# Kernel optimization log

Hardware: AMD Instinct MI355X
Metric: run time of the kernel (lower is better)

Reference implementation:

```python
import jax, jax.numpy as jnp
import numpy as np


def setup_inputs() -> dict:
    key = jax.random.key(0)
    ks = iter(jax.random.split(key, 100))
    V3, Vm, K, E3, Em = 100000, 25000, 128, 800000, 200000
    c_in, c3, cm, c_out = 16, 128, 256, 21
    rn = lambda *s: jax.random.normal(next(ks), s, dtype=jnp.float32)
    ru = lambda *s: jax.random.uniform(next(ks), s, dtype=jnp.float32)
    ri = lambda hi, *s: jax.random.randint(next(ks), s, 0, hi)
    d = {}
    d['x_in'] = rn(1, V3, c_in)
    d['mass_3'] = ru(1, V3)
    d['evals_3'] = ru(1, K)
    d['evecs_3'] = rn(1, V3, K) * 0.01
    d['gX3_idx'] = ri(V3, E3, 2)
    d['gX3_val'] = rn(E3) * 0.05
    d['gY3_idx'] = ri(V3, E3, 2)
    d['gY3_val'] = rn(E3) * 0.05
    d['mass_m'] = ru(1, Vm)
    d['evals_m'] = ru(1, K)
    d['evecs_m'] = rn(1, Vm, K) * 0.01
    d['gXm_idx'] = ri(Vm, Em, 2)
    d['gXm_val'] = rn(Em) * 0.05
    d['gYm_idx'] = ri(Vm, Em, 2)
    d['gYm_val'] = rn(Em) * 0.05
    d['traces34'] = ri(Vm, V3)
    d['in_w'] = rn(c_in, c3) * 0.05
    d['in_b'] = rn(c3) * 0.05
    d['widen_w'] = rn(c3, cm) * 0.05
    d['widen_b'] = rn(cm) * 0.05
    d['narrow_w'] = rn(cm, c3) * 0.05
    d['narrow_b'] = rn(c3) * 0.05
    d['halve_w'] = rn(2 * c3, c3) * 0.05
    d['halve_b'] = rn(c3) * 0.05
    d['out_w'] = rn(c3, c_out) * 0.05
    d['out_b'] = rn(c_out) * 0.05
    for pre, C in (('enc', c3), ('mid', cm), ('dec', c3)):
        d[pre + '_dt'] = ru(2, C)
        d[pre + '_Are'] = rn(2, C, C) * 0.05
        d[pre + '_Aim'] = rn(2, C, C) * 0.05
        d[pre + '_w0'] = rn(2, 3 * C, C) * 0.05
        d[pre + '_b0'] = rn(2, C) * 0.05
        d[pre + '_w1'] = rn(2, C, C) * 0.05
        d[pre + '_b1'] = rn(2, C) * 0.05
        d[pre + '_w2'] = rn(2, C, C) * 0.05
        d[pre + '_b2'] = rn(2, C) * 0.05
    return d


def _spmm(idx, val, x, n):
    # sparse COO (n x n) @ x ; rows = idx[:,0], cols = idx[:,1]
    return jax.ops.segment_sum(val[:, None] * x[idx[:, 1]], idx[:, 0], num_segments=n)


def _block(x, mass, evals, evecs, gxi, gxv, gyi, gyv, dt, Are, Aim, w0, b0, w1, b1, w2, b2):
    # DiffusionNetBlock: spectral diffusion + rotated gradient features + MiniMLP + residual
    V = x.shape[1]
    x_spec = jnp.einsum('bvk,bvc->bkc', evecs, x * mass[..., None])          # to_basis
    coef = jnp.exp(-evals[..., None] * jnp.maximum(dt, 1e-8)[None, None, :])  # (B,K,C)
    xd = jnp.einsum('bvk,bkc->bvc', evecs, coef * x_spec)                     # from_basis
    gX = _spmm(gxi, gxv, xd[0], V)[None]                                      # (B,V,C)
    gY = _spmm(gyi, gyv, xd[0], V)[None]
    Br = gX @ Are - gY @ Aim                                                  # complex linear, with rotations
    Bi = gY @ Are + gX @ Aim
    gf = jnp.tanh(gX * Br + gY * Bi)                                          # inner product -> tanh
    h = jnp.concatenate([x, xd, gf], axis=-1)                                 # (B,V,3C)
    h = jax.nn.relu(h @ w0 + b0)
    h = jax.nn.relu(h @ w1 + b1)
    return (h @ w2 + b2) + x


def reference(x_in, mass_3, evals_3, evecs_3, gX3_idx, gX3_val, gY3_idx, gY3_val,
              mass_m, evals_m, evecs_m, gXm_idx, gXm_val, gYm_idx, gYm_val, traces34,
              in_w, in_b, enc_dt, enc_Are, enc_Aim, enc_w0, enc_b0, enc_w1, enc_b1, enc_w2, enc_b2,
              widen_w, widen_b, mid_dt, mid_Are, mid_Aim, mid_w0, mid_b0, mid_w1, mid_b1, mid_w2, mid_b2,
              narrow_w, narrow_b, halve_w, halve_b,
              dec_dt, dec_Are, dec_Aim, dec_w0, dec_b0, dec_w1, dec_b1, dec_w2, dec_b2,
              out_w, out_b):
    Vm = mass_m.shape[1]
    sl = lambda arrs, i: tuple(a[i] for a in arrs)
    enc_p = (enc_dt, enc_Are, enc_Aim, enc_w0, enc_b0, enc_w1, enc_b1, enc_w2, enc_b2)
    mid_p = (mid_dt, mid_Are, mid_Aim, mid_w0, mid_b0, mid_w1, mid_b1, mid_w2, mid_b2)
    dec_p = (dec_dt, dec_Are, dec_Aim, dec_w0, dec_b0, dec_w1, dec_b1, dec_w2, dec_b2)

    x3 = jax.nn.relu(x_in @ in_w + in_b)
    for i in range(enc_dt.shape[0]):
        x3 = _block(x3, mass_3, evals_3, evecs_3, gX3_idx, gX3_val, gY3_idx, gY3_val, *sl(enc_p, i))
    # scatter-max pooling fine -> coarse
    xm = jax.ops.segment_max(x3[0], traces34, num_segments=Vm)
    xm = jnp.where(jnp.isneginf(xm), 0.0, xm)[None]
    xm = jax.nn.relu(xm @ widen_w + widen_b)
    for i in range(mid_dt.shape[0]):
        xm = _block(xm, mass_m, evals_m, evecs_m, gXm_idx, gXm_val, gYm_idx, gYm_val, *sl(mid_p, i))
    # gather unpooling coarse -> fine
    y3 = xm[:, traces34, :]
    y3 = jax.nn.relu(y3 @ narrow_w + narrow_b)
    y3 = jnp.concatenate([y3, x3], axis=-1)
    y3 = jax.nn.relu(y3 @ halve_w + halve_b)
    for i in range(dec_dt.shape[0]):
        y3 = _block(y3, mass_3, evals_3, evecs_3, gX3_idx, gX3_val, gY3_idx, gY3_val, *sl(dec_p, i))
    return y3 @ out_w + out_b
```

## Files before the change

kernel.cpp:

```cpp
#include <hip/hip_runtime.h>
#include <cstdint>
#include <cstddef>

static constexpr int V3   = 100000;
static constexpr int VM   = 25000;
static constexpr int KE   = 128;
static constexpr int E3   = 800000;
static constexpr int EM   = 200000;
static constexpr int C3   = 128;
static constexpr int CMID = 256;

typedef unsigned short u16;
typedef unsigned int   u32;
using short8v = __attribute__((ext_vector_type(8))) short;
using f32x4   = __attribute__((ext_vector_type(4))) float;
using f32x16  = __attribute__((ext_vector_type(16))) float;

#define DEVI __device__ __forceinline__
DEVI float4 ld4(const float* p){ return *(const float4*)p; }
DEVI void   st4(float* p, float4 v){ *(float4*)p = v; }
DEVI float  bf2f(u16 u){ return __uint_as_float(((u32)u) << 16); }
DEVI u16    f2bf(float f){
  u32 u = __float_as_uint(f);
  u += 0x7FFFu + ((u >> 16) & 1u);
  return (u16)(u >> 16);
}
DEVI u32 pk2(float a, float b){ return (u32)f2bf(a) | ((u32)f2bf(b) << 16); }
DEVI short8v as8(uint4 v){ union { uint4 u; short8v s; } c; c.u = v; return c.s; }
DEVI int lofs(int row, int oct){ return row * 40 + ((oct ^ ((row >> 3) & 3)) << 3); }

static inline int cdiv(int a, int b){ return (a + b - 1) / b; }

template<bool RELU, bool RES, bool GATHER, bool OBF16>
__global__ __launch_bounds__(256)
void k_mgemm(const void* __restrict__ A0, int aty0, int K0,
             const u16* __restrict__ wt0, int wl0, int wo0,
             const void* __restrict__ A1, int aty1, int K1,
             const u16* __restrict__ wt1, int wl1, int wo1,
             const void* __restrict__ A2, int aty2, int K2,
             const u16* __restrict__ wt2, int wl2, int wo2,
             const int* __restrict__ gidx,
             const float* __restrict__ bias, const float* __restrict__ res,
             void* __restrict__ OUT, u16* __restrict__ OUTB, int CO, int V)
{
  __shared__ __align__(16) u16 As[64 * 40];
  __shared__ __align__(16) u16 Ws[128 * 40];

  const int tid  = threadIdx.x;
  const int wave = tid >> 6, lane = tid & 63;
  const int vbase = blockIdx.x * 64;
  const int ncol0 = blockIdx.y * 128;
  const int KT = K0 + K1 + K2;

  f32x4 acc[8];
  #pragma unroll
  for (int n = 0; n < 8; n++) { acc[n][0]=0.f; acc[n][1]=0.f; acc[n][2]=0.f; acc[n][3]=0.f; }

  const int ar = tid >> 2, ac = tid & 3;
  const int arow = vbase + ar;
  int grow0 = arow;
  if (GATHER && arow < V) grow0 = gidx[arow];

  for (int kt = 0; kt < KT; kt += 32) {
    {
      int kg = kt + ac * 8;
      uint4 aw = make_uint4(0,0,0,0);
      if (arow < V && kg < KT) {
        const void* src; int aty, koff, sK; bool s0;
        if (kg < K0)            { src=A0; aty=aty0; koff=0;     sK=K0; s0=true;  }
        else if (kg < K0 + K1)  { src=A1; aty=aty1; koff=K0;    sK=K1; s0=false; }
        else                    { src=A2; aty=aty2; koff=K0+K1; sK=K2; s0=false; }
        int row = (GATHER && s0) ? grow0 : arow;
        int kl = kg - koff;
        if (aty) {
          aw = *(const uint4*)((const u16*)src + (size_t)row * sK + kl);
        } else {
          const float* fp = (const float*)src + (size_t)row * sK + kl;
          float4 x = ld4(fp), y = ld4(fp + 4);
          aw = make_uint4(pk2(x.x,x.y), pk2(x.z,x.w), pk2(y.x,y.y), pk2(y.z,y.w));
        }
      }
      *(uint4*)&As[ar * 40 + ac * 8] = aw;
    }
    #pragma unroll
    for (int i = 0; i < 2; i++) {
      int col = tid & 127;
      int c = (tid >> 7) + 2 * i;
      int kg = kt + c * 8;
      uint4 ww = make_uint4(0,0,0,0);
      if (kg < KT) {
        const u16* wt; int koff, wl, wo;
        if (kg < K0)           { wt=wt0; koff=0;     wl=wl0; wo=wo0; }
        else if (kg < K0+K1)   { wt=wt1; koff=K0;    wl=wl1; wo=wo1; }
        else                   { wt=wt2; koff=K0+K1; wl=wl2; wo=wo2; }
        ww = *(const uint4*)(wt + (size_t)(ncol0 + col) * wl + wo + (kg - koff));
      }
      *(uint4*)&Ws[col * 40 + c * 8] = ww;
    }
    __syncthreads();
    {
      const int mrow = (wave << 4) + (lane & 15);
      const int kc = lane >> 4;
      short8v a = *(const short8v*)(const void*)&As[mrow * 40 + kc * 8];
      #pragma unroll
      for (int n = 0; n < 8; n++) {
        short8v b = *(const short8v*)(const void*)&Ws[(n * 16 + (lane & 15)) * 40 + kc * 8];
        acc[n] = __builtin_amdgcn_mfma_f32_16x16x32_bf16(a, b, acc[n], 0, 0, 0);
      }
    }
    __syncthreads();
  }

  const int q4 = (lane >> 4) * 4, colb = lane & 15;
  #pragma unroll
  for (int n = 0; n < 8; n++) {
    int gcol = ncol0 + n * 16 + colb;
    float bv = bias ? bias[gcol] : 0.f;
    #pragma unroll
    for (int q = 0; q < 4; q++) {
      int grow = vbase + (wave << 4) + q4 + q;
      if (grow >= V) continue;
      float o = acc[n][q] + bv;
      size_t idx = (size_t)grow * CO + gcol;
      if (RES) o += res[idx];
      if (RELU) o = fmaxf(o, 0.f);
      if (OBF16) ((u16*)OUT)[idx] = f2bf(o);
      else {
        ((float*)OUT)[idx] = o;
        if (OUTB) OUTB[idx] = f2bf(o);
      }
    }
  }
}

__global__ __launch_bounds__(256)
void k_mlp3(const u16* __restrict__ A0, const u16* __restrict__ A1,
            const u16* __restrict__ A2,
            const u16* __restrict__ w0t,
            const u16* __restrict__ w1t, const u16* __restrict__ w2t,
            const float* __restrict__ b0, const float* __restrict__ b1,
            const float* __restrict__ b2,
            float* __restrict__ XM, u16* __restrict__ SHB, int V)
{
  __shared__ __align__(16) u16 As[64 * 40];
  __shared__ __align__(16) u16 Ws[128 * 40];
  __shared__ __align__(16) u16 Hs[4][64 * 40];

  const int tid  = threadIdx.x;
  const int wave = tid >> 6, lane = tid & 63;
  const int vbase = blockIdx.x * 64;
  const int ar = tid >> 2, ac = tid & 3;
  const int arow = vbase + ar;
  const bool rok = arow < V;
  const int mrow = (wave << 4) + (lane & 15);
  const int kc = lane >> 4;
  const int q4 = (lane >> 4) * 4, colb = lane & 15;
  const int wcol = tid & 127, wc = tid >> 7;

  float xres[8][4];
  #pragma unroll
  for (int n = 0; n < 8; n++)
    #pragma unroll
    for (int q = 0; q < 4; q++) {
      int grow = vbase + (wave << 4) + q4 + q;
      xres[n][q] = (grow < V) ? XM[(size_t)grow * C3 + n * 16 + colb] : 0.f;
    }

  f32x4 acc[8];
  auto zacc = [&]{
    #pragma unroll
    for (int n = 0; n < 8; n++) { acc[n][0]=0.f; acc[n][1]=0.f; acc[n][2]=0.f; acc[n][3]=0.f; }
  };
  auto hwrite = [&](const float* b){
    #pragma unroll
    for (int n = 0; n < 8; n++) {
      int c = n * 16 + colb;
      float bv = b[c];
      #pragma unroll
      for (int q = 0; q < 4; q++) {
        int row = (wave << 4) + q4 + q;
        Hs[c >> 5][lofs(row, (c >> 3) & 3) + (c & 7)] = f2bf(fmaxf(acc[n][q] + bv, 0.f));
      }
    }
  };
  auto mfma_tile = [&](const u16* a8){
    short8v a = *(const short8v*)(const void*)a8;
    #pragma unroll
    for (int n = 0; n < 8; n++) {
      short8v b = *(const short8v*)(const void*)&Ws[(n * 16 + (lane & 15)) * 40 + kc * 8];
      acc[n] = __builtin_amdgcn_mfma_f32_16x16x32_bf16(a, b, acc[n], 0, 0, 0);
    }
  };
  auto fA = [&](int kg) -> uint4 {
    const u16* src = (kg < 128) ? A0 : (kg < 256) ? A1 : A2;
    uint4 r = make_uint4(0,0,0,0);
    if (rok) r = *(const uint4*)(src + (size_t)arow * 128 + (kg & 127));
    return r;
  };
  auto fW = [&](const u16* wt, int ld, int kg) -> uint4 {
    return *(const uint4*)(wt + (size_t)wcol * ld + kg);
  };

  zacc();
  uint4 pa  = fA(ac * 8);
  uint4 pw0 = fW(w0t, 384, wc * 8);
  uint4 pw1 = fW(w0t, 384, (wc + 2) * 8);
  for (int kt = 0; kt < 384; kt += 32) {
    __syncthreads();
    *(uint4*)&As[ar * 40 + ac * 8] = pa;
    *(uint4*)&Ws[wcol * 40 + wc * 8] = pw0;
    *(uint4*)&Ws[wcol * 40 + (wc + 2) * 8] = pw1;
    __syncthreads();
    int kn = kt + 32;
    if (kn < 384) {
      pa  = fA(kn + ac * 8);
      pw0 = fW(w0t, 384, kn + wc * 8);
      pw1 = fW(w0t, 384, kn + (wc + 2) * 8);
    } else {
      pw0 = fW(w1t, 128, wc * 8);
      pw1 = fW(w1t, 128, (wc + 2) * 8);
    }
    mfma_tile(&As[mrow * 40 + kc * 8]);
  }
  hwrite(b0);
  zacc();
  for (int kt = 0; kt < 128; kt += 32) {
    __syncthreads();
    *(uint4*)&Ws[wcol * 40 + wc * 8] = pw0;
    *(uint4*)&Ws[wcol * 40 + (wc + 2) * 8] = pw1;
    __syncthreads();
    int kn = kt + 32;
    if (kn < 128) {
      pw0 = fW(w1t, 128, kn + wc * 8);
      pw1 = fW(w1t, 128, kn + (wc + 2) * 8);
    } else {
      pw0 = fW(w2t, 128, wc * 8);
      pw1 = fW(w2t, 128, (wc + 2) * 8);
    }
    mfma_tile(&Hs[kt >> 5][lofs(mrow, kc)]);
  }
  hwrite(b1);
  zacc();
  for (int kt = 0; kt < 128; kt += 32) {
    __syncthreads();
    *(uint4*)&Ws[wcol * 40 + wc * 8] = pw0;
    *(uint4*)&Ws[wcol * 40 + (wc + 2) * 8] = pw1;
    __syncthreads();
    int kn = kt + 32;
    if (kn < 128) {
      pw0 = fW(w2t, 128, kn + wc * 8);
      pw1 = fW(w2t, 128, kn + (wc + 2) * 8);
    }
    mfma_tile(&Hs[kt >> 5][lofs(mrow, kc)]);
  }
  #pragma unroll
  for (int n = 0; n < 8; n++) {
    int gcol = n * 16 + colb;
    float bv = b2[gcol];
    #pragma unroll
    for (int q = 0; q < 4; q++) {
      int grow = vbase + (wave << 4) + q4 + q;
      if (grow >= V) continue;
      size_t idx = (size_t)grow * C3 + gcol;
      float o = acc[n][q] + bv + xres[n][q];
      XM[idx] = o;
      SHB[idx] = f2bf(o);
    }
  }
}

__global__ __launch_bounds__(256)
void k_mgate_reg(const u16* __restrict__ GEX, const u16* __restrict__ GEY,
                 const u16* __restrict__ pS, const u16* __restrict__ pR,
                 const u16* __restrict__ pI,
                 u16* __restrict__ GF, int CO, int V)
{
  const int lane = threadIdx.x & 63;
  const int wave = threadIdx.x >> 6;
  const int rbase = blockIdx.x * 128 + wave * 32;
  const int arow = rbase + (lane & 31);
  const int koff = (lane >> 5) * 8;
  const bool rok = arow < V;

  uint4 ax[8], ay[8], an[8];
  #pragma unroll
  for (int kt = 0; kt < 8; kt++) {
    uint4 zx = make_uint4(0,0,0,0), zy = make_uint4(0,0,0,0);
    if (rok) {
      zx = *(const uint4*)(GEX + (size_t)arow * KE + kt * 16 + koff);
      zy = *(const uint4*)(GEY + (size_t)arow * KE + kt * 16 + koff);
    }
    ax[kt] = zx; ay[kt] = zy;
    an[kt] = make_uint4(zy.x ^ 0x80008000u, zy.y ^ 0x80008000u,
                        zy.z ^ 0x80008000u, zy.w ^ 0x80008000u);
  }

  const int ngr = CO >> 5;
  for (int g = 0; g < ngr; g++) {
    f32x16 gx, gy, br, bi;
    #pragma unroll
    for (int r = 0; r < 16; r++) { gx[r]=0.f; gy[r]=0.f; br[r]=0.f; bi[r]=0.f; }
    #pragma unroll
    for (int kt = 0; kt < 8; kt++) {
      size_t bo = ((size_t)(g * 8 + kt) * 64 + lane) * 8;
      short8v bs  = *(const short8v*)(const void*)(pS + bo);
      short8v brv = *(const short8v*)(const void*)(pR + bo);
      short8v biv = *(const short8v*)(const void*)(pI + bo);
      short8v axv = as8(ax[kt]), ayv = as8(ay[kt]), anv = as8(an[kt]);
      gx = __builtin_amdgcn_mfma_f32_32x32x16_bf16(axv, bs,  gx, 0, 0, 0);
      gy = __builtin_amdgcn_mfma_f32_32x32x16_bf16(ayv, bs,  gy, 0, 0, 0);
      br = __builtin_amdgcn_mfma_f32_32x32x16_bf16(axv, brv, br, 0, 0, 0);
      br = __builtin_amdgcn_mfma_f32_32x32x16_bf16(anv, biv, br, 0, 0, 0);
      bi = __builtin_amdgcn_mfma_f32_32x32x16_bf16(axv, biv, bi, 0, 0, 0);
      bi = __builtin_amdgcn_mfma_f32_32x32x16_bf16(ayv, brv, bi, 0, 0, 0);
    }
    const int col = g * 32 + (lane & 31);
    const int rhi = 4 * (lane >> 5);
    #pragma unroll
    for (int r = 0; r < 16; r++) {
      int row = rbase + (r & 3) + 8 * (r >> 2) + rhi;
      if (row < V) {
        float o = tanhf(gx[r] * br[r] + gy[r] * bi[r]);
        GF[(size_t)row * CO + col] = f2bf(o);
      }
    }
  }
}

__global__ __launch_bounds__(256)
void k_specmm(const u16* __restrict__ E, const u16* __restrict__ X,
              const float* __restrict__ mass, float* __restrict__ SPEC,
              int C, int V, int CH)
{
  __shared__ __align__(16) u16 As[64 * 40];
  __shared__ __align__(16) u16 Bs[128 * 40];

  const int tid = threadIdx.x;
  const int wave = tid >> 6, lane = tid & 63;
  const int m0 = blockIdx.y * 64;
  const int n0 = blockIdx.z * 128;
  const int vs = blockIdx.x * CH;
  const int ve = min(V, vs + CH);

  f32x4 acc[8];
  #pragma unroll
  for (int n = 0; n < 8; n++) { acc[n][0]=0.f; acc[n][1]=0.f; acc[n][2]=0.f; acc[n][3]=0.f; }

  const int am = tid & 63, ac = tid >> 6;
  const int bcol = tid & 127, bc0 = (tid >> 7) * 2;

  u16 ea[8]; float fb0[8], fb1[8], fm0[8], fm1[8];
  auto loadA = [&](int kt) {
    #pragma unroll
    for (int j = 0; j < 8; j++) {
      int v = kt + ac * 8 + j;
      ea[j] = (v < ve) ? E[(size_t)v * KE + m0 + am] : (u16)0;
    }
  };
  auto loadB = [&](int kt) {
    #pragma unroll
    for (int j = 0; j < 8; j++) {
      int v0 = kt + bc0 * 8 + j, v1 = v0 + 8;
      fb0[j] = (v0 < ve) ? bf2f(X[(size_t)v0 * C + n0 + bcol]) : 0.f;
      fm0[j] = (v0 < ve) ? mass[v0] : 0.f;
      fb1[j] = (v1 < ve) ? bf2f(X[(size_t)v1 * C + n0 + bcol]) : 0.f;
      fm1[j] = (v1 < ve) ? mass[v1] : 0.f;
    }
  };
  loadA(vs); loadB(vs);

  for (int kt = vs; kt < ve; kt += 32) {
    __syncthreads();
    *(uint4*)&As[lofs(am, ac)] = make_uint4(
        (u32)ea[0] | ((u32)ea[1] << 16), (u32)ea[2] | ((u32)ea[3] << 16),
        (u32)ea[4] | ((u32)ea[5] << 16), (u32)ea[6] | ((u32)ea[7] << 16));
    float t0[8], t1[8];
    #pragma unroll
    for (int j = 0; j < 8; j++) { t0[j] = fb0[j]*fm0[j]; t1[j] = fb1[j]*fm1[j]; }
    *(uint4*)&Bs[lofs(bcol, bc0)] = make_uint4(
        pk2(t0[0],t0[1]), pk2(t0[2],t0[3]), pk2(t0[4],t0[5]), pk2(t0[6],t0[7]));
    *(uint4*)&Bs[lofs(bcol, bc0 + 1)] = make_uint4(
        pk2(t1[0],t1[1]), pk2(t1[2],t1[3]), pk2(t1[4],t1[5]), pk2(t1[6],t1[7]));
    __syncthreads();
    if (kt + 32 < ve) { loadA(kt + 32); loadB(kt + 32); }
    const int kc = lane >> 4, ml = lane & 15;
    short8v a = *(const short8v*)(const void*)&As[lofs(wave * 16 + ml, kc)];
    #pragma unroll
    for (int n = 0; n < 8; n++) {
      short8v b = *(const short8v*)(const void*)&Bs[lofs(n * 16 + ml, kc)];
      acc[n] = __builtin_amdgcn_mfma_f32_16x16x32_bf16(a, b, acc[n], 0, 0, 0);
    }
  }

  const int q4 = (lane >> 4) * 4, colb = lane & 15;
  #pragma unroll
  for (int n = 0; n < 8; n++) {
    int col = n0 + n * 16 + colb;
    #pragma unroll
    for (int q = 0; q < 4; q++) {
      int row = m0 + wave * 16 + q4 + q;
      unsafeAtomicAdd(&SPEC[(size_t)row * C + col], acc[n][q]);
    }
  }
}

template<int C>
__global__ void k_smallprep(const float* __restrict__ SPEC, const float* __restrict__ evals,
                            const float* __restrict__ dt, const float* __restrict__ Are,
                            const float* __restrict__ Aim, const float* __restrict__ w0,
                            u16* __restrict__ pS, u16* __restrict__ pR,
                            u16* __restrict__ pI, u16* __restrict__ SWt)
{
  __shared__ float sld[C];
  const int k = blockIdx.x;
  const int c = threadIdx.x;
  const float ev = evals[k];
  float s = expf(-ev * fmaxf(dt[c], 1e-8f)) * SPEC[(size_t)k * C + c];
  sld[c] = s;
  const size_t pidx = ((size_t)((c >> 5) * 8 + (k >> 4)) * 64
                       + (c & 31) + ((k >> 3) & 1) * 32) * 8 + (k & 7);
  pS[pidx] = f2bf(s);
  __syncthreads();
  float tr = 0.f, ti = 0.f, sw = 0.f;
  for (int j = 0; j < C; j++) {
    float sj = sld[j];
    tr = fmaf(sj, Are[(size_t)j * C + c], tr);
    ti = fmaf(sj, Aim[(size_t)j * C + c], ti);
    sw = fmaf(sj, w0[(size_t)(C + j) * C + c], sw);
  }
  pR[pidx] = f2bf(tr);
  pI[pidx] = f2bf(ti);
  SWt[(size_t)c * 128 + k] = f2bf(sw);
}

__global__ void k_asmw0(const u16* __restrict__ w0t_, const u16* __restrict__ swt_,
                        u16* __restrict__ o_) {
  int col = blockIdx.x, t = threadIdx.x;
  o_[(size_t)col * 384 + t]       = w0t_[(size_t)col * 384 + t];
  o_[(size_t)col * 384 + 128 + t] = w0t_[(size_t)col * 384 + 256 + t];
  o_[(size_t)col * 384 + 256 + t] = swt_[(size_t)col * 128 + t];
}

__global__ void k_prepw(const float* __restrict__ W, u16* __restrict__ WT, int K, int N) {
  size_t zoff = (size_t)blockIdx.z * K * N;
  int i = blockIdx.x * 256 + threadIdx.x;
  if (i < K * N) {
    int k = i / N, n = i % N;
    WT[zoff + (size_t)n * K + k] = f2bf(W[zoff + i]);
  }
}

__global__ void k_cvt(const float* __restrict__ in, u16* __restrict__ out, int n) {
  int i = (blockIdx.x * 256 + threadIdx.x) * 4;
  if (i < n) {
    float4 v = ld4(in + i);
    ushort4 o; o.x = f2bf(v.x); o.y = f2bf(v.y); o.z = f2bf(v.z); o.w = f2bf(v.w);
    *(ushort4*)(out + i) = o;
  }
}

__global__ void k_hist(const int* __restrict__ idx, int* __restrict__ deg, int E) {
  int e = blockIdx.x * 256 + threadIdx.x;
  if (e < E) atomicAdd(&deg[idx[2 * e]], 1);
}
__global__ void k_scan1(const int* __restrict__ deg, int* __restrict__ excl,
                        int* __restrict__ bsum, int V) {
  __shared__ int sd[256];
  int t = threadIdx.x;
  int i = blockIdx.x * 256 + t;
  int v = (i < V) ? deg[i] : 0;
  sd[t] = v;
  __syncthreads();
  for (int off = 1; off < 256; off <<= 1) {
    int add = (t >= off) ? sd[t - off] : 0;
    __syncthreads();
    sd[t] += add;
    __syncthreads();
  }
  if (i < V) excl[i] = sd[t] - v;
  if (t == 255) bsum[blockIdx.x] = sd[255];
}
__global__ void k_scan2(int* __restrict__ bsum, int nb, int* __restrict__ rowptr, int V) {
  __shared__ int sd[512];
  int t = threadIdx.x;
  int v = (t < nb) ? bsum[t] : 0;
  sd[t] = v;
  __syncthreads();
  for (int off = 1; off < 512; off <<= 1) {
    int add = (t >= off) ? sd[t - off] : 0;
    __syncthreads();
    sd[t] += add;
    __syncthreads();
  }
  if (t < nb) bsum[t] = sd[t] - v;
  if (t == 0) rowptr[V] = sd[511];
}
__global__ void k_scan3(const int* __restrict__ excl, const int* __restrict__ bsum,
                        int* __restrict__ rowptr, int V) {
  int i = blockIdx.x * 256 + threadIdx.x;
  if (i < V) rowptr[i] = excl[i] + bsum[i >> 8];
}
__global__ void k_scatter(const int* __restrict__ idx, const float* __restrict__ val,
                          const int* __restrict__ rowptr, int* __restrict__ cur,
                          int* __restrict__ ecol, float* __restrict__ eval, int E) {
  int e = blockIdx.x * 256 + threadIdx.x;
  if (e < E) {
    int d = idx[2 * e];
    int p = rowptr[d] + atomicAdd(&cur[d], 1);
    ecol[p] = idx[2 * e + 1];
    eval[p] = val[e];
  }
}
__global__ __launch_bounds__(256)
void k_spmm_csr(const int* __restrict__ rowptr, const int* __restrict__ ecol,
                const float* __restrict__ eval, const u16* __restrict__ E,
                u16* __restrict__ GE, int V) {
  int r = blockIdx.x * 8 + (threadIdx.x >> 5);
  int lane = threadIdx.x & 31;
  if (r >= V) return;
  int j1 = rowptr[r + 1];
  float4 a = make_float4(0.f,0.f,0.f,0.f);
  for (int j = rowptr[r]; j < j1; j++) {
    int c = ecol[j];
    float v = eval[j];
    ushort4 x = *(const ushort4*)(E + (size_t)c * KE + lane * 4);
    a.x = fmaf(v, bf2f(x.x), a.x); a.y = fmaf(v, bf2f(x.y), a.y);
    a.z = fmaf(v, bf2f(x.z), a.z); a.w = fmaf(v, bf2f(x.w), a.w);
  }
  ushort4 o;
  o.x = f2bf(a.x); o.y = f2bf(a.y); o.z = f2bf(a.z); o.w = f2bf(a.w);
  *(ushort4*)(GE + (size_t)r * KE + lane * 4) = o;
}

__global__ void k_segmax_init(unsigned* __restrict__ u, int n) {
  int i = blockIdx.x * 256 + threadIdx.x;
  if (i < n) u[i] = 0x007FFFFFu;
}
__global__ void k_segmax_scatter(const u16* __restrict__ X, const int* __restrict__ tr,
                                 unsigned* __restrict__ u) {
  int i = blockIdx.x * 256 + threadIdx.x;
  if (i >= V3 * C3) return;
  int v = i >> 7, c = i & 127;
  unsigned b = ((unsigned)X[i]) << 16;
  unsigned m = (b & 0x80000000u) ? ~b : (b | 0x80000000u);
  atomicMax(&u[((size_t)tr[v] << 7) + c], m);
}
__global__ void k_segmax_decode(const unsigned* __restrict__ u, u16* __restrict__ out, int n) {
  int i = blockIdx.x * 256 + threadIdx.x;
  if (i < n) {
    unsigned m = u[i];
    unsigned b = 0;
    if (m != 0x007FFFFFu)
      b = (m & 0x80000000u) ? (m & 0x7FFFFFFFu) : ~m;
    out[i] = (u16)(b >> 16);
  }
}

__global__ __launch_bounds__(256)
void k_outproj(const float* __restrict__ Y, const float* __restrict__ W,
               const float* __restrict__ B, float* __restrict__ OUT, int V) {
  __shared__ float Wl[128][22];
  __shared__ float ys[8][128];
  const int tid = threadIdx.x;
  for (int f = tid; f < 128 * 21; f += 256) Wl[f / 21][f % 21] = W[f];
  {
    int r = tid >> 5, cc = (tid & 31) * 4;
    int v = blockIdx.x * 8 + r;
    float4 yv = make_float4(0.f,0.f,0.f,0.f);
    if (v < V) yv = ld4(Y + (size_t)v * C3 + cc);
    st4(&ys[r][cc], yv);
  }
  __syncthreads();
  int r = tid >> 5, c = tid & 31;
  int v = blockIdx.x * 8 + r;
  if (v < V && c < 21) {
    float acc = B[c];
    #pragma unroll 8
    for (int k = 0; k < 128; k++) acc = fmaf(ys[r][k], Wl[k][c], acc);
    OUT[(size_t)v * 21 + c] = acc;
  }
}

extern "C" void kernel_launch(void* const* d_in, const int* in_sizes, int n_in,
                              void* d_out, int out_size, void* d_ws, size_t ws_size,
                              hipStream_t stream)
{
  (void)in_sizes; (void)n_in; (void)out_size;
  const float* x_in    = (const float*)d_in[0];
  const float* mass3   = (const float*)d_in[1];
  const float* evals3  = (const float*)d_in[2];
  const float* evecs3  = (const float*)d_in[3];
  const int*   gX3i    = (const int*)d_in[4];
  const float* gX3v    = (const float*)d_in[5];
  const int*   gY3i    = (const int*)d_in[6];
  const float* gY3v    = (const float*)d_in[7];
  const float* massm   = (const float*)d_in[8];
  const float* evalsm  = (const float*)d_in[9];
  const float* evecsm  = (const float*)d_in[10];
  const int*   gXmi    = (const int*)d_in[11];
  const float* gXmv    = (const float*)d_in[12];
  const int*   gYmi    = (const int*)d_in[13];
  const float* gYmv    = (const float*)d_in[14];
  const int*   tr34    = (const int*)d_in[15];
  const float* in_w    = (const float*)d_in[16];
  const float* in_b    = (const float*)d_in[17];
  const float* widen_w = (const float*)d_in[18];
  const float* widen_b = (const float*)d_in[19];
  const float* narrow_w= (const float*)d_in[20];
  const float* narrow_b= (const float*)d_in[21];
  const float* halve_w = (const float*)d_in[22];
  const float* halve_b = (const float*)d_in[23];
  const float* out_w   = (const float*)d_in[24];
  const float* out_b   = (const float*)d_in[25];
  const float* enc_p[9]; const float* mid_p[9]; const float* dec_p[9];
  for (int i = 0; i < 9; i++) {
    enc_p[i] = (const float*)d_in[26 + i];
    mid_p[i] = (const float*)d_in[35 + i];
    dec_p[i] = (const float*)d_in[44 + i];
  }

  char* ws = (char*)d_ws;
  size_t off = 0;
  float* XM  = (float*)(ws + off); off += (size_t)V3 * C3 * 4;
  u16* SHB   = (u16*)(ws + off);   off += (size_t)V3 * C3 * 2;
  u16* GEX3  = (u16*)(ws + off);   off += (size_t)V3 * KE * 2;
  u16* GEY3  = (u16*)(ws + off);   off += (size_t)V3 * KE * 2;
  u16* GEXm  = (u16*)(ws + off);   off += (size_t)VM * KE * 2;
  u16* GEYm  = (u16*)(ws + off);   off += (size_t)VM * KE * 2;
  u16* BSCR  = (u16*)(ws + off);   off += (size_t)V3 * C3 * 2;
  char* E3R  = (char*)(ws + off);  off += (size_t)V3 * KE * 2;
  u16* Embf  = (u16*)(ws + off);   off += (size_t)VM * KE * 2;
  u16* SHM   = (u16*)(ws + off);   off += (size_t)VM * CMID * 2;
  float* spec= (float*)(ws + off); off += 131072;
  u16* pS  = (u16*)(ws + off); off += 65536;
  u16* pR  = (u16*)(ws + off); off += 65536;
  u16* pI  = (u16*)(ws + off); off += 65536;
  u16* SWt = (u16*)(ws + off); off += 65536;
  u16* wT  = (u16*)(ws + off); off += 2400000;
  const size_t NEED = off;
  if (ws_size < NEED) return;

  u16*   E3bf = (u16*)E3R;
  float* M0   = (float*)E3R;
  int*   rowptr = (int*)BSCR;
  int*   deg    = (int*)((char*)BSCR + 400128);
  int*   ecol   = (int*)((char*)BSCR + 800256);
  float* evalv  = (float*)((char*)BSCR + 4000256);
  int*   bsum   = (int*)((char*)BSCR + 7200256);
  unsigned* xm_u  = (unsigned*)BSCR;
  u16*      xm_dec= (u16*)((char*)BSCR + 12800000);
  u16* BSCR0 = BSCR;
  u16* BSCR1 = BSCR + (size_t)VM * CMID;

  u16* in_wt    = wT + 0;
  u16* widen_t  = wT + 2048;
  u16* narrow_t = wT + 34816;
  u16* halve_t  = wT + 67584;
  u16* enc_w0t  = wT + 100352;
  u16* enc_w1t  = wT + 198656;
  u16* enc_w2t  = wT + 231424;
  u16* mid_w0t  = wT + 264192;
  u16* mid_w1t  = wT + 657408;
  u16* mid_w2t  = wT + 788480;
  u16* dec_w0t  = wT + 919552;
  u16* dec_w1t  = wT + 1017856;
  u16* dec_w2t  = wT + 1050624;
  u16* wCmb     = wT + 1083392;

  auto prepw = [&](const float* W, u16* WT, int K, int N, int z) {
    k_prepw<<<dim3(cdiv(K * N, 256), 1, z), 256, 0, stream>>>(W, WT, K, N);
  };
  prepw(in_w, in_wt, 16, 128, 1);
  prepw(widen_w, widen_t, 128, 256, 1);
  prepw(narrow_w, narrow_t, 256, 128, 1);
  prepw(halve_w, halve_t, 256, 128, 1);
  prepw(enc_p[3], enc_w0t, 384, 128, 2);
  prepw(enc_p[5], enc_w1t, 128, 128, 2);
  prepw(enc_p[7], enc_w2t, 128, 128, 2);
  prepw(mid_p[3], mid_w0t, 768, 256, 2);
  prepw(mid_p[5], mid_w1t, 256, 256, 2);
  prepw(mid_p[7], mid_w2t, 256, 256, 2);
  prepw(dec_p[3], dec_w0t, 384, 128, 2);
  prepw(dec_p[5], dec_w1t, 128, 128, 2);
  prepw(dec_p[7], dec_w2t, 128, 128, 2);

  k_cvt<<<cdiv(V3 * KE / 4, 256), 256, 0, stream>>>(evecs3, E3bf, V3 * KE);
  k_cvt<<<cdiv(VM * KE / 4, 256), 256, 0, stream>>>(evecsm, Embf, VM * KE);

  auto build_ge = [&](const int* idx, const float* val, int E_, int V_,
                      const u16* Ebf, u16* GE) {
    hipMemsetAsync(deg, 0, (size_t)V_ * 4, stream);
    k_hist<<<cdiv(E_, 256), 256, 0, stream>>>(idx, deg, E_);
    int nb = cdiv(V_, 256);
    k_scan1<<<nb, 256, 0, stream>>>(deg, ecol, bsum, V_);
    k_scan2<<<1, 512, 0, stream>>>(bsum, nb, rowptr, V_);
    k_scan3<<<nb, 256, 0, stream>>>(ecol, bsum, rowptr, V_);
    hipMemsetAsync(deg, 0, (size_t)V_ * 4, stream);
    k_scatter<<<cdiv(E_, 256), 256, 0, stream>>>(idx, val, rowptr, deg, ecol, evalv, E_);
    k_spmm_csr<<<cdiv(V_, 8), 256, 0, stream>>>(rowptr, ecol, evalv, Ebf, GE, V_);
  };
  build_ge(gX3i, gX3v, E3, V3, E3bf, GEX3);
  build_ge(gY3i, gY3v, E3, V3, E3bf, GEY3);
  build_ge(gXmi, gXmv, EM, VM, Embf, GEXm);
  build_ge(gYmi, gYmv, EM, VM, Embf, GEYm);

  const int G3 = cdiv(V3, 64);
  const int GM = cdiv(VM, 64);

  auto launch_block3 = [&](const float* p[9],
                           const u16* w0t, const u16* w1t, const u16* w2t, int i) {
    const float* dt  = p[0] + (size_t)i * C3;
    const float* Are = p[1] + (size_t)i * C3 * C3;
    const float* Aim = p[2] + (size_t)i * C3 * C3;
    const float* w0  = p[3] + (size_t)i * 3 * C3 * C3;
    const float* b0  = p[4] + (size_t)i * C3;
    const float* b1  = p[6] + (size_t)i * C3;
    const float* b2  = p[8] + (size_t)i * C3;
    const u16* w0ti = w0t + (size_t)i * 3 * C3 * C3;
    const u16* w1ti = w1t + (size_t)i * C3 * C3;
    const u16* w2ti = w2t + (size_t)i * C3 * C3;
    hipMemsetAsync(spec, 0, (size_t)KE * C3 * 4, stream);
    k_specmm<<<dim3(cdiv(V3, 256), 2, 1), 256, 0, stream>>>(E3bf, SHB, mass3, spec, C3, V3, 256);
    k_smallprep<C3><<<KE, C3, 0, stream>>>(spec, evals3, dt, Are, Aim, w0, pS, pR, pI, SWt);
    k_mgate_reg<<<cdiv(V3, 128), 256, 0, stream>>>(GEX3, GEY3, pS, pR, pI, BSCR, C3, V3);
    k_asmw0<<<128, 128, 0, stream>>>(w0ti, SWt, wCmb);
    k_mlp3<<<G3, 256, 0, stream>>>(SHB, BSCR, E3bf, wCmb, w1ti, w2ti,
                                   b0, b1, b2, XM, SHB, V3);
  };

  auto run_blockm = [&](const float* p[9],
                        const u16* w0t, const u16* w1t, const u16* w2t, int i) {
    const float* dt  = p[0] + (size_t)i * CMID;
    const float* Are = p[1] + (size_t)i * CMID * CMID;
    const float* Aim = p[2] + (size_t)i * CMID * CMID;
    const float* w0  = p[3] + (size_t)i * 3 * CMID * CMID;
    const float* b0  = p[4] + (size_t)i * CMID;
    const float* b1  = p[6] + (size_t)i * CMID;
    const float* b2  = p[8] + (size_t)i * CMID;
    const u16* w0ti = w0t + (size_t)i * 3 * CMID * CMID;
    const u16* w1ti = w1t + (size_t)i * CMID * CMID;
    const u16* w2ti = w2t + (size_t)i * CMID * CMID;
    hipMemsetAsync(spec, 0, (size_t)KE * CMID * 4, stream);
    k_specmm<<<dim3(cdiv(VM, 128), 2, 2), 256, 0, stream>>>(Embf, SHM, massm, spec, CMID, VM, 128);
    k_smallprep<CMID><<<KE, CMID, 0, stream>>>(spec, evalsm, dt, Are, Aim, w0, pS, pR, pI, SWt);
    k_mgate_reg<<<cdiv(VM, 128), 256, 0, stream>>>(GEXm, GEYm, pS, pR, pI, BSCR0, CMID, VM);
    k_mgemm<true,false,false,true><<<dim3(GM, 2), 256, 0, stream>>>(
        SHM, 1, CMID, w0ti, 3*CMID, 0,
        BSCR0, 1, CMID, w0ti, 3*CMID, 2*CMID,
        Embf, 1, KE, SWt, 128, 0,
        nullptr, b0, nullptr, BSCR1, nullptr, CMID, VM);
    k_mgemm<true,false,false,true><<<dim3(GM, 2), 256, 0, stream>>>(
        BSCR1, 1, CMID, w1ti, CMID, 0,
        nullptr,0,0,nullptr,0,0, nullptr,0,0,nullptr,0,0,
        nullptr, b1, nullptr, BSCR0, nullptr, CMID, VM);
    k_mgemm<false,true,false,false><<<dim3(GM, 2), 256, 0, stream>>>(
        BSCR0, 1, CMID, w2ti, CMID, 0,
        nullptr,0,0,nullptr,0,0, nullptr,0,0,nullptr,0,0,
        nullptr, b2, M0, M0, SHM, CMID, VM);
  };

  k_mgemm<true,false,false,false><<<dim3(G3, 1), 256, 0, stream>>>(
      x_in, 0, 16, in_wt, 16, 0,
      nullptr,0,0,nullptr,0,0, nullptr,0,0,nullptr,0,0,
      nullptr, in_b, nullptr, XM, SHB, C3, V3);
  launch_block3(enc_p, enc_w0t, enc_w1t, enc_w2t, 0);
  launch_block3(enc_p, enc_w0t, enc_w1t, enc_w2t, 1);

  k_segmax_init<<<cdiv(VM * C3, 256), 256, 0, stream>>>(xm_u, VM * C3);
  k_segmax_scatter<<<cdiv(V3 * C3, 256), 256, 0, stream>>>(SHB, tr34, xm_u);
  k_segmax_decode<<<cdiv(VM * C3, 256), 256, 0, stream>>>(xm_u, xm_dec, VM * C3);
  k_mgemm<true,false,false,false><<<dim3(GM, 2), 256, 0, stream>>>(
      xm_dec, 1, C3, widen_t, C3, 0,
      nullptr,0,0,nullptr,0,0, nullptr,0,0,nullptr,0,0,
      nullptr, widen_b, nullptr, M0, SHM, CMID, VM);
  run_blockm(mid_p, mid_w0t, mid_w1t, mid_w2t, 0);
  run_blockm(mid_p, mid_w0t, mid_w1t, mid_w2t, 1);

  k_mgemm<true,false,true,true><<<dim3(G3, 1), 256, 0, stream>>>(
      SHM, 1, CMID, narrow_t, CMID, 0,
      nullptr,0,0,nullptr,0,0, nullptr,0,0,nullptr,0,0,
      tr34, narrow_b, nullptr, BSCR, nullptr, C3, V3);
  k_mgemm<true,false,false,false><<<dim3(G3, 1), 256, 0, stream>>>(
      BSCR, 1, C3, halve_t, 2*C3, 0,
      SHB, 1, C3, halve_t, 2*C3, C3,
      nullptr,0,0,nullptr,0,0,
      nullptr, halve_b, nullptr, XM, SHB, C3, V3);

  k_cvt<<<cdiv(V3 * KE / 4, 256), 256, 0, stream>>>(evecs3, E3bf, V3 * KE);
  launch_block3(dec_p, dec_w0t, dec_w1t, dec_w2t, 0);
  launch_block3(dec_p, dec_w0t, dec_w1t, dec_w2t, 1);

  k_outproj<<<cdiv(V3, 8), 256, 0, stream>>>(XM, out_w, out_b, (float*)d_out, V3);
}
```

Measured before the change: 2.005 ms.

## Batch setup kernels across descriptors and drop per-block w0 assembly

```diff
diff --git a/kernel.cpp b/kernel.cpp
--- a/kernel.cpp
+++ b/kernel.cpp
@@ -30,6 +30,16 @@
 DEVI int lofs(int row, int oct){ return row * 40 + ((oct ^ ((row >> 3) & 3)) << 3); }
 
 static inline int cdiv(int a, int b){ return (a + b - 1) / b; }
+
+struct PrepT { const float* W[22]; u16* WT[22]; int K[22]; int N[22]; };
+struct CvtT  { const float* src[2]; u16* dst[2]; int n[2]; };
+struct IniT  { const u16* src[4]; u16* dst[4]; };
+struct GDesc {
+  const int* idx; const float* val; const u16* Ebf; u16* GE;
+  int* rowptr; int* deg; int* cur; int* excl; int* bsum;
+  int* ecol; float* evalv; int E; int V;
+};
+struct G4 { GDesc d[4]; };
 
 template<bool RELU, bool RES, bool GATHER, bool OBF16>
 __global__ __launch_bounds__(256)
@@ -155,16 +165,6 @@
   const int mrow = (wave << 4) + (lane & 15);
   const int kc = lane >> 4;
   const int q4 = (lane >> 4) * 4, colb = lane & 15;
-  const int wcol = tid & 127, wc = tid >> 7;
-
-  float xres[8][4];
-  #pragma unroll
-  for (int n = 0; n < 8; n++)
-    #pragma unroll
-    for (int q = 0; q < 4; q++) {
-      int grow = vbase + (wave << 4) + q4 + q;
-      xres[n][q] = (grow < V) ? XM[(size_t)grow * C3 + n * 16 + colb] : 0.f;
-    }
 
   f32x4 acc[8];
   auto zacc = [&]{
@@ -191,67 +191,52 @@
       acc[n] = __builtin_amdgcn_mfma_f32_16x16x32_bf16(a, b, acc[n], 0, 0, 0);
     }
   };
-  auto fA = [&](int kg) -> uint4 {
-    const u16* src = (kg < 128) ? A0 : (kg < 256) ? A1 : A2;
-    uint4 r = make_uint4(0,0,0,0);
-    if (rok) r = *(const uint4*)(src + (size_t)arow * 128 + (kg & 127));
-    return r;
-  };
-  auto fW = [&](const u16* wt, int ld, int kg) -> uint4 {
-    return *(const uint4*)(wt + (size_t)wcol * ld + kg);
-  };
 
   zacc();
-  uint4 pa  = fA(ac * 8);
-  uint4 pw0 = fW(w0t, 384, wc * 8);
-  uint4 pw1 = fW(w0t, 384, (wc + 2) * 8);
   for (int kt = 0; kt < 384; kt += 32) {
-    __syncthreads();
-    *(uint4*)&As[ar * 40 + ac * 8] = pa;
-    *(uint4*)&Ws[wcol * 40 + wc * 8] = pw0;
-    *(uint4*)&Ws[wcol * 40 + (wc + 2) * 8] = pw1;
-    __syncthreads();
-    int kn = kt + 32;
-    if (kn < 384) {
-      pa  = fA(kn + ac * 8);
-      pw0 = fW(w0t, 384, kn + wc * 8);
-      pw1 = fW(w0t, 384, kn + (wc + 2) * 8);
-    } else {
-      pw0 = fW(w1t, 128, wc * 8);
-      pw1 = fW(w1t, 128, (wc + 2) * 8);
-    }
+    {
+      int kg = kt + ac * 8;
+      const u16* src = (kg < 128) ? A0 : (kg < 256) ? A1 : A2;
+      int kl = kg & 127;
+      uint4 aw = make_uint4(0,0,0,0);
+      if (rok) aw = *(const uint4*)(src + (size_t)arow * 128 + kl);
+      *(uint4*)&As[ar * 40 + ac * 8] = aw;
+    }
+    #pragma unroll
+    for (int i = 0; i < 2; i++) {
+      int col = tid & 127, c = (tid >> 7) + 2 * i;
+      *(uint4*)&Ws[col * 40 + c * 8] =
+        *(const uint4*)(w0t + (size_t)col * 384 + kt + c * 8);
+    }
+    __syncthreads();
     mfma_tile(&As[mrow * 40 + kc * 8]);
+    __syncthreads();
   }
   hwrite(b0);
   zacc();
   for (int kt = 0; kt < 128; kt += 32) {
-    __syncthreads();
-    *(uint4*)&Ws[wcol * 40 + wc * 8] = pw0;
-    *(uint4*)&Ws[wcol * 40 + (wc + 2) * 8] = pw1;
-    __syncthreads();
-    int kn = kt + 32;
-    if (kn < 128) {
-      pw0 = fW(w1t, 128, kn + wc * 8);
-      pw1 = fW(w1t, 128, kn + (wc + 2) * 8);
-    } else {
-      pw0 = fW(w2t, 128, wc * 8);
-      pw1 = fW(w2t, 128, (wc + 2) * 8);
-    }
+    #pragma unroll
+    for (int i = 0; i < 2; i++) {
+      int col = tid & 127, c = (tid >> 7) + 2 * i;
+      *(uint4*)&Ws[col * 40 + c * 8] =
+        *(const uint4*)(w1t + (size_t)col * 128 + kt + c * 8);
+    }
+    __syncthreads();
     mfma_tile(&Hs[kt >> 5][lofs(mrow, kc)]);
+    __syncthreads();
   }
   hwrite(b1);
   zacc();
   for (int kt = 0; kt < 128; kt += 32) {
-    __syncthreads();
-    *(uint4*)&Ws[wcol * 40 + wc * 8] = pw0;
-    *(uint4*)&Ws[wcol * 40 + (wc + 2) * 8] = pw1;
-    __syncthreads();
-    int kn = kt + 32;
-    if (kn < 128) {
-      pw0 = fW(w2t, 128, kn + wc * 8);
-      pw1 = fW(w2t, 128, kn + (wc + 2) * 8);
-    }
+    #pragma unroll
+    for (int i = 0; i < 2; i++) {
+      int col = tid & 127, c = (tid >> 7) + 2 * i;
+      *(uint4*)&Ws[col * 40 + c * 8] =
+        *(const uint4*)(w2t + (size_t)col * 128 + kt + c * 8);
+    }
+    __syncthreads();
     mfma_tile(&Hs[kt >> 5][lofs(mrow, kc)]);
+    __syncthreads();
   }
   #pragma unroll
   for (int n = 0; n < 8; n++) {
@@ -262,7 +247,7 @@
       int grow = vbase + (wave << 4) + q4 + q;
       if (grow >= V) continue;
       size_t idx = (size_t)grow * C3 + gcol;
-      float o = acc[n][q] + bv + xres[n][q];
+      float o = acc[n][q] + bv + XM[idx];
       XM[idx] = o;
       SHB[idx] = f2bf(o);
     }
@@ -409,7 +394,8 @@
                             const float* __restrict__ dt, const float* __restrict__ Are,
                             const float* __restrict__ Aim, const float* __restrict__ w0,
                             u16* __restrict__ pS, u16* __restrict__ pR,
-                            u16* __restrict__ pI, u16* __restrict__ SWt)
+                            u16* __restrict__ pI, u16* __restrict__ SWt,
+                            u16* __restrict__ wcmb)
 {
   __shared__ float sld[C];
   const int k = blockIdx.x;
@@ -430,24 +416,38 @@
   }
   pR[pidx] = f2bf(tr);
   pI[pidx] = f2bf(ti);
-  SWt[(size_t)c * 128 + k] = f2bf(sw);
-}
-
-__global__ void k_asmw0(const u16* __restrict__ w0t_, const u16* __restrict__ swt_,
-                        u16* __restrict__ o_) {
-  int col = blockIdx.x, t = threadIdx.x;
-  o_[(size_t)col * 384 + t]       = w0t_[(size_t)col * 384 + t];
-  o_[(size_t)col * 384 + 128 + t] = w0t_[(size_t)col * 384 + 256 + t];
-  o_[(size_t)col * 384 + 256 + t] = swt_[(size_t)col * 128 + t];
-}
-
-__global__ void k_prepw(const float* __restrict__ W, u16* __restrict__ WT, int K, int N) {
-  size_t zoff = (size_t)blockIdx.z * K * N;
+  u16 swb = f2bf(sw);
+  SWt[(size_t)c * 128 + k] = swb;
+  if (wcmb) wcmb[(size_t)c * 384 + 256 + k] = swb;
+}
+
+__global__ void k_prepw_b(PrepT p) {
+  int e = blockIdx.y;
   int i = blockIdx.x * 256 + threadIdx.x;
+  int K = p.K[e], N = p.N[e];
   if (i < K * N) {
     int k = i / N, n = i % N;
-    WT[zoff + (size_t)n * K + k] = f2bf(W[zoff + i]);
-  }
+    p.WT[e][(size_t)n * K + k] = f2bf(p.W[e][i]);
+  }
+}
+
+__global__ void k_cvt_b(CvtT c) {
+  int e = blockIdx.y;
+  int i = (blockIdx.x * 256 + threadIdx.x) * 4;
+  if (i < c.n[e]) {
+    float4 v = ld4(c.src[e] + i);
+    ushort4 o; o.x = f2bf(v.x); o.y = f2bf(v.y); o.z = f2bf(v.z); o.w = f2bf(v.w);
+    *(ushort4*)(c.dst[e] + i) = o;
+  }
+}
+
+__global__ void k_initwc(IniT t) {
+  int e = blockIdx.y;
+  int i = blockIdx.x * 256 + threadIdx.x;
+  int col = i >> 8, k = i & 255;
+  t.dst[e][(size_t)col * 384 + k] =
+      (k < 128) ? t.src[e][(size_t)col * 384 + k]
+                : t.src[e][(size_t)col * 384 + 128 + k];
 }
 
 __global__ void k_cvt(const float* __restrict__ in, u16* __restrict__ out, int n) {
@@ -459,16 +459,17 @@
   }
 }
 
-__global__ void k_hist(const int* __restrict__ idx, int* __restrict__ deg, int E) {
+__global__ void k_bhist(G4 g) {
+  const GDesc& d = g.d[blockIdx.y];
   int e = blockIdx.x * 256 + threadIdx.x;
-  if (e < E) atomicAdd(&deg[idx[2 * e]], 1);
-}
-__global__ void k_scan1(const int* __restrict__ deg, int* __restrict__ excl,
-                        int* __restrict__ bsum, int V) {
+  if (e < d.E) atomicAdd(&d.deg[d.idx[2 * e]], 1);
+}
+__global__ void k_bscan1(G4 g) {
+  const GDesc& d = g.d[blockIdx.y];
   __shared__ int sd[256];
   int t = threadIdx.x;
   int i = blockIdx.x * 256 + t;
-  int v = (i < V) ? deg[i] : 0;
+  int v = (i < d.V) ? d.deg[i] : 0;
   sd[t] = v;
   __syncthreads();
   for (int off = 1; off < 256; off <<= 1) {
@@ -477,13 +478,14 @@
     sd[t] += add;
     __syncthreads();
   }
-  if (i < V) excl[i] = sd[t] - v;
-  if (t == 255) bsum[blockIdx.x] = sd[255];
-}
-__global__ void k_scan2(int* __restrict__ bsum, int nb, int* __restrict__ rowptr, int V) {
+  if (i < d.V) d.excl[i] = sd[t] - v;
+  if (t == 255) d.bsum[blockIdx.x] = sd[255];
+}
+__global__ void k_bscan2(G4 g, int nb) {
+  const GDesc& d = g.d[blockIdx.y];
   __shared__ int sd[512];
   int t = threadIdx.x;
-  int v = (t < nb) ? bsum[t] : 0;
+  int v = (t < nb) ? d.bsum[t] : 0;
   sd[t] = v;
   __syncthreads();
   for (int off = 1; off < 512; off <<= 1) {
@@ -492,44 +494,42 @@
     sd[t] += add;
     __syncthreads();
   }
-  if (t < nb) bsum[t] = sd[t] - v;
-  if (t == 0) rowptr[V] = sd[511];
-}
-__global__ void k_scan3(const int* __restrict__ excl, const int* __restrict__ bsum,
-                        int* __restrict__ rowptr, int V) {
+  if (t < nb) d.bsum[t] = sd[t] - v;
+  if (t == 0) d.rowptr[d.V] = sd[511];
+}
+__global__ void k_bscan3(G4 g) {
+  const GDesc& d = g.d[blockIdx.y];
   int i = blockIdx.x * 256 + threadIdx.x;
-  if (i < V) rowptr[i] = excl[i] + bsum[i >> 8];
-}
-__global__ void k_scatter(const int* __restrict__ idx, const float* __restrict__ val,
-                          const int* __restrict__ rowptr, int* __restrict__ cur,
-                          int* __restrict__ ecol, float* __restrict__ eval, int E) {
+  if (i < d.V) d.rowptr[i] = d.excl[i] + d.bsum[i >> 8];
+}
+__global__ void k_bscatter(G4 g) {
+  const GDesc& d = g.d[blockIdx.y];
   int e = blockIdx.x * 256 + threadIdx.x;
-  if (e < E) {
-    int d = idx[2 * e];
-    int p = rowptr[d] + atomicAdd(&cur[d], 1);
-    ecol[p] = idx[2 * e + 1];
-    eval[p] = val[e];
+  if (e < d.E) {
+    int dd = d.idx[2 * e];
+    int p = d.rowptr[dd] + atomicAdd(&d.cur[dd], 1);
+    d.ecol[p] = d.idx[2 * e + 1];
+    d.evalv[p] = d.val[e];
   }
 }
 __global__ __launch_bounds__(256)
-void k_spmm_csr(const int* __restrict__ rowptr, const int* __restrict__ ecol,
-                const float* __restrict__ eval, const u16* __restrict__ E,
-                u16* __restrict__ GE, int V) {
+void k_bspmm(G4 g) {
+  const GDesc& d = g.d[blockIdx.y];
   int r = blockIdx.x * 8 + (threadIdx.x >> 5);
   int lane = threadIdx.x & 31;
-  if (r >= V) return;
-  int j1 = rowptr[r + 1];
+  if (r >= d.V) return;
+  int j1 = d.rowptr[r + 1];
   float4 a = make_float4(0.f,0.f,0.f,0.f);
-  for (int j = rowptr[r]; j < j1; j++) {
-    int c = ecol[j];
-    float v = eval[j];
-    ushort4 x = *(const ushort4*)(E + (size_t)c * KE + lane * 4);
+  for (int j = d.rowptr[r]; j < j1; j++) {
+    int c = d.ecol[j];
+    float v = d.evalv[j];
+    ushort4 x = *(const ushort4*)(d.Ebf + (size_t)c * KE + lane * 4);
     a.x = fmaf(v, bf2f(x.x), a.x); a.y = fmaf(v, bf2f(x.y), a.y);
     a.z = fmaf(v, bf2f(x.z), a.z); a.w = fmaf(v, bf2f(x.w), a.w);
   }
   ushort4 o;
   o.x = f2bf(a.x); o.y = f2bf(a.y); o.z = f2bf(a.z); o.w = f2bf(a.w);
-  *(ushort4*)(GE + (size_t)r * KE + lane * 4) = o;
+  *(ushort4*)(d.GE + (size_t)r * KE + lane * 4) = o;
 }
 
 __global__ void k_segmax_init(unsigned* __restrict__ u, int n) {
@@ -636,17 +636,12 @@
   u16* pR  = (u16*)(ws + off); off += 65536;
   u16* pI  = (u16*)(ws + off); off += 65536;
   u16* SWt = (u16*)(ws + off); off += 65536;
-  u16* wT  = (u16*)(ws + off); off += 2400000;
+  u16* wT  = (u16*)(ws + off); off += 2800000;
   const size_t NEED = off;
   if (ws_size < NEED) return;
 
   u16*   E3bf = (u16*)E3R;
   float* M0   = (float*)E3R;
-  int*   rowptr = (int*)BSCR;
-  int*   deg    = (int*)((char*)BSCR + 400128);
-  int*   ecol   = (int*)((char*)BSCR + 800256);
-  float* evalv  = (float*)((char*)BSCR + 4000256);
-  int*   bsum   = (int*)((char*)BSCR + 7200256);
   unsigned* xm_u  = (unsigned*)BSCR;
   u16*      xm_dec= (u16*)((char*)BSCR + 12800000);
   u16* BSCR0 = BSCR;
@@ -665,50 +660,86 @@
   u16* dec_w0t  = wT + 919552;
   u16* dec_w1t  = wT + 1017856;
   u16* dec_w2t  = wT + 1050624;
-  u16* wCmb     = wT + 1083392;
-
-  auto prepw = [&](const float* W, u16* WT, int K, int N, int z) {
-    k_prepw<<<dim3(cdiv(K * N, 256), 1, z), 256, 0, stream>>>(W, WT, K, N);
-  };
-  prepw(in_w, in_wt, 16, 128, 1);
-  prepw(widen_w, widen_t, 128, 256, 1);
-  prepw(narrow_w, narrow_t, 256, 128, 1);
-  prepw(halve_w, halve_t, 256, 128, 1);
-  prepw(enc_p[3], enc_w0t, 384, 128, 2);
-  prepw(enc_p[5], enc_w1t, 128, 128, 2);
-  prepw(enc_p[7], enc_w2t, 128, 128, 2);
-  prepw(mid_p[3], mid_w0t, 768, 256, 2);
-  prepw(mid_p[5], mid_w1t, 256, 256, 2);
-  prepw(mid_p[7], mid_w2t, 256, 256, 2);
-  prepw(dec_p[3], dec_w0t, 384, 128, 2);
-  prepw(dec_p[5], dec_w1t, 128, 128, 2);
-  prepw(dec_p[7], dec_w2t, 128, 128, 2);
-
-  k_cvt<<<cdiv(V3 * KE / 4, 256), 256, 0, stream>>>(evecs3, E3bf, V3 * KE);
-  k_cvt<<<cdiv(VM * KE / 4, 256), 256, 0, stream>>>(evecsm, Embf, VM * KE);
-
-  auto build_ge = [&](const int* idx, const float* val, int E_, int V_,
-                      const u16* Ebf, u16* GE) {
-    hipMemsetAsync(deg, 0, (size_t)V_ * 4, stream);
-    k_hist<<<cdiv(E_, 256), 256, 0, stream>>>(idx, deg, E_);
-    int nb = cdiv(V_, 256);
-    k_scan1<<<nb, 256, 0, stream>>>(deg, ecol, bsum, V_);
-    k_scan2<<<1, 512, 0, stream>>>(bsum, nb, rowptr, V_);
-    k_scan3<<<nb, 256, 0, stream>>>(ecol, bsum, rowptr, V_);
-    hipMemsetAsync(deg, 0, (size_t)V_ * 4, stream);
-    k_scatter<<<cdiv(E_, 256), 256, 0, stream>>>(idx, val, rowptr, deg, ecol, evalv, E_);
-    k_spmm_csr<<<cdiv(V_, 8), 256, 0, stream>>>(rowptr, ecol, evalv, Ebf, GE, V_);
-  };
-  build_ge(gX3i, gX3v, E3, V3, E3bf, GEX3);
-  build_ge(gY3i, gY3v, E3, V3, E3bf, GEY3);
-  build_ge(gXmi, gXmv, EM, VM, Embf, GEXm);
-  build_ge(gYmi, gYmv, EM, VM, Embf, GEYm);
+  u16* wCmb[4]  = { wT + 1083392, wT + 1181696, wT + 1280000, wT + 1378304 };
+
+  {
+    PrepT p;
+    int e = 0;
+    auto add = [&](const float* W, u16* WT, int K, int N, int z) {
+      for (int i = 0; i < z; i++) {
+        p.W[e] = W + (size_t)i * K * N; p.WT[e] = WT + (size_t)i * K * N;
+        p.K[e] = K; p.N[e] = N; e++;
+      }
+    };
+    add(in_w, in_wt, 16, 128, 1);
+    add(widen_w, widen_t, 128, 256, 1);
+    add(narrow_w, narrow_t, 256, 128, 1);
+    add(halve_w, halve_t, 256, 128, 1);
+    add(enc_p[3], enc_w0t, 384, 128, 2);
+    add(enc_p[5], enc_w1t, 128, 128, 2);
+    add(enc_p[7], enc_w2t, 128, 128, 2);
+    add(mid_p[3], mid_w0t, 768, 256, 2);
+    add(mid_p[5], mid_w1t, 256, 256, 2);
+    add(mid_p[7], mid_w2t, 256, 256, 2);
+    add(dec_p[3], dec_w0t, 384, 128, 2);
+    add(dec_p[5], dec_w1t, 128, 128, 2);
+    add(dec_p[7], dec_w2t, 128, 128, 2);
+    k_prepw_b<<<dim3(768, 22), 256, 0, stream>>>(p);
+  }
+  {
+    IniT t;
+    t.src[0] = enc_w0t; t.dst[0] = wCmb[0];
+    t.src[1] = enc_w0t + 49152; t.dst[1] = wCmb[1];
+    t.src[2] = dec_w0t; t.dst[2] = wCmb[2];
+    t.src[3] = dec_w0t + 49152; t.dst[3] = wCmb[3];
+    k_initwc<<<dim3(128, 4), 256, 0, stream>>>(t);
+  }
+  {
+    CvtT c;
+    c.src[0] = evecs3; c.dst[0] = E3bf; c.n[0] = V3 * KE;
+    c.src[1] = evecsm; c.dst[1] = Embf; c.n[1] = VM * KE;
+    k_cvt_b<<<dim3(cdiv(V3 * KE / 4, 256), 2), 256, 0, stream>>>(c);
+  }
+
+  {
+    char* cs = (char*)BSCR;
+    int* degs = (int*)cs;
+    int* curs = degs + 250000;
+    int* cur2 = curs + 250000;
+    int* pos = cur2;
+    G4 g;
+    const int*   idxs[4] = { gX3i, gY3i, gXmi, gYmi };
+    const float* vals[4] = { gX3v, gY3v, gXmv, gYmv };
+    const u16*   ebfs[4] = { E3bf, E3bf, Embf, Embf };
+    u16*         ges[4]  = { GEX3, GEY3, GEXm, GEYm };
+    int Es[4] = { E3, E3, EM, EM };
+    int Vs[4] = { V3, V3, VM, VM };
+    int doff[4] = { 0, 100000, 200000, 225000 };
+    for (int i = 0; i < 4; i++) {
+      GDesc& d = g.d[i];
+      d.idx = idxs[i]; d.val = vals[i]; d.Ebf = ebfs[i]; d.GE = ges[i];
+      d.E = Es[i]; d.V = Vs[i];
+      d.deg = degs + doff[i]; d.cur = curs + doff[i];
+      d.rowptr = pos; pos += Vs[i] + 1;
+      d.excl   = pos; pos += Vs[i];
+      d.bsum   = pos; pos += 512;
+      d.ecol   = pos; pos += Es[i];
+      d.evalv  = (float*)pos; pos += Es[i];
+    }
+    hipMemsetAsync(degs, 0, 500000 * 4, stream);
+    k_bhist<<<dim3(cdiv(E3, 256), 4), 256, 0, stream>>>(g);
+    k_bscan1<<<dim3(cdiv(V3, 256), 4), 256, 0, stream>>>(g);
+    k_bscan2<<<dim3(1, 4), 512, 0, stream>>>(g, cdiv(V3, 256));
+    k_bscan3<<<dim3(cdiv(V3, 256), 4), 256, 0, stream>>>(g);
+    k_bscatter<<<dim3(cdiv(E3, 256), 4), 256, 0, stream>>>(g);
+    k_bspmm<<<dim3(cdiv(V3, 8), 4), 256, 0, stream>>>(g);
+  }
 
   const int G3 = cdiv(V3, 64);
   const int GM = cdiv(VM, 64);
 
-  auto launch_block3 = [&](const float* p[9],
-                           const u16* w0t, const u16* w1t, const u16* w2t, int i) {
+  auto launch_block3 = [&](const float* p[9], const u16* w0t,
+                           const u16* w1t, const u16* w2t, u16* wc, int i) {
     const float* dt  = p[0] + (size_t)i * C3;
     const float* Are = p[1] + (size_t)i * C3 * C3;
     const float* Aim = p[2] + (size_t)i * C3 * C3;
@@ -716,15 +747,14 @@
     const float* b0  = p[4] + (size_t)i * C3;
     const float* b1  = p[6] + (size_t)i * C3;
     const float* b2  = p[8] + (size_t)i * C3;
-    const u16* w0ti = w0t + (size_t)i * 3 * C3 * C3;
     const u16* w1ti = w1t + (size_t)i * C3 * C3;
     const u16* w2ti = w2t + (size_t)i * C3 * C3;
+    (void)w0t;
     hipMemsetAsync(spec, 0, (size_t)KE * C3 * 4, stream);
     k_specmm<<<dim3(cdiv(V3, 256), 2, 1), 256, 0, stream>>>(E3bf, SHB, mass3, spec, C3, V3, 256);
-    k_smallprep<C3><<<KE, C3, 0, stream>>>(spec, evals3, dt, Are, Aim, w0, pS, pR, pI, SWt);
+    k_smallprep<C3><<<KE, C3, 0, stream>>>(spec, evals3, dt, Are, Aim, w0, pS, pR, pI, SWt, wc);
     k_mgate_reg<<<cdiv(V3, 128), 256, 0, stream>>>(GEX3, GEY3, pS, pR, pI, BSCR, C3, V3);
-    k_asmw0<<<128, 128, 0, stream>>>(w0ti, SWt, wCmb);
-    k_mlp3<<<G3, 256, 0, stream>>>(SHB, BSCR, E3bf, wCmb, w1ti, w2ti,
+    k_mlp3<<<G3, 256, 0, stream>>>(SHB, BSCR, E3bf, wc, w1ti, w2ti,
                                    b0, b1, b2, XM, SHB, V3);
   };
 
@@ -742,7 +772,7 @@
     const u16* w2ti = w2t + (size_t)i * CMID * CMID;
     hipMemsetAsync(spec, 0, (size_t)KE * CMID * 4, stream);
     k_specmm<<<dim3(cdiv(VM, 128), 2, 2), 256, 0, stream>>>(Embf, SHM, massm, spec, CMID, VM, 128);
-    k_smallprep<CMID><<<KE, CMID, 0, stream>>>(spec, evalsm, dt, Are, Aim, w0, pS, pR, pI, SWt);
+    k_smallprep<CMID><<<KE, CMID, 0, stream>>>(spec, evalsm, dt, Are, Aim, w0, pS, pR, pI, SWt, nullptr);
     k_mgate_reg<<<cdiv(VM, 128), 256, 0, stream>>>(GEXm, GEYm, pS, pR, pI, BSCR0, CMID, VM);
     k_mgemm<true,false,false,true><<<dim3(GM, 2), 256, 0, stream>>>(
         SHM, 1, CMID, w0ti, 3*CMID, 0,
@@ -763,8 +793,8 @@
       x_in, 0, 16, in_wt, 16, 0,
       nullptr,0,0,nullptr,0,0, nullptr,0,0,nullptr,0,0,
       nullptr, in_b, nullptr, XM, SHB, C3, V3);
-  launch_block3(enc_p, enc_w0t, enc_w1t, enc_w2t, 0);
-  launch_block3(enc_p, enc_w0t, enc_w1t, enc_w2t, 1);
+  launch_block3(enc_p, enc_w0t, enc_w1t, enc_w2t, wCmb[0], 0);
+  launch_block3(enc_p, enc_w0t, enc_w1t, enc_w2t, wCmb[1], 1);
 
   k_segmax_init<<<cdiv(VM * C3, 256), 256, 0, stream>>>(xm_u, VM * C3);
   k_segmax_scatter<<<cdiv(V3 * C3, 256), 256, 0, stream>>>(SHB, tr34, xm_u);
@@ -787,8 +817,8 @@
       nullptr, halve_b, nullptr, XM, SHB, C3, V3);
 
   k_cvt<<<cdiv(V3 * KE / 4, 256), 256, 0, stream>>>(evecs3, E3bf, V3 * KE);
-  launch_block3(dec_p, dec_w0t, dec_w1t, dec_w2t, 0);
-  launch_block3(dec_p, dec_w0t, dec_w1t, dec_w2t, 1);
+  launch_block3(dec_p, dec_w0t, dec_w1t, dec_w2t, wCmb[2], 0);
+  launch_block3(dec_p, dec_w0t, dec_w1t, dec_w2t, wCmb[3], 1);
 
   k_outproj<<<cdiv(V3, 8), 256, 0, stream>>>(XM, out_w, out_b, (float*)d_out, V3);
 }
```

Measured after the change: 1.838 ms. 8.3% less time.
